# Performance work log

Measured on AMD Instinct MI355X. Metric: run time of the kernel, lower is better.

The kernel has to match this reference:

```python
import jax, jax.numpy as jnp
import numpy as np

B, DIN, DOUT, NC = 8192, 4096, 4096, 64


def setup_inputs() -> dict:
    key = jax.random.key(0)
    k1, k2, k3, k4, k5 = jax.random.split(key, 5)
    x = jax.random.normal(k1, (B, DIN), dtype=jnp.float32)
    cluster = jax.random.uniform(k2, (B, NC), dtype=jnp.float32)
    weight = jax.random.uniform(k3, (DIN, DOUT), dtype=jnp.float32,
                                minval=-0.25, maxval=0.25)
    # torch init is ones; perturb slightly so the modulation is non-trivial
    style_L = 1.0 + 0.1 * jax.random.normal(k4, (NC, DIN), dtype=jnp.float32)
    style_R = 1.0 + 0.1 * jax.random.normal(k5, (NC, DOUT), dtype=jnp.float32)
    return {"x": x, "cluster": cluster, "weight": weight,
            "style_L": style_L, "style_R": style_R}


def reference(x, cluster, weight, style_L, style_R):
    # tmp_L: (B, din), tmp_R: (B, dout)
    tmp_L = cluster @ style_L
    tmp_R = cluster @ style_R
    # Algebraically identical to (weight * outer(tmp_L, tmp_R)) applied per
    # sample: out[b,o] = sum_i x[b,i]*tmpL[b,i]*W[i,o]*tmpR[b,o].
    # Factorized form avoids the (B, din, dout) intermediate.
    return ((x * tmp_L) @ weight) * tmp_R
```

## Files before the change

### kernel.cpp

```cpp
#include <hip/hip_runtime.h>
#include <cstdint>

#define BB   8192
#define DIN  4096
#define DOUT 4096
#define NCL  64

typedef __bf16 bf16;
typedef __attribute__((ext_vector_type(8))) __bf16 bf16x8;
typedef __attribute__((ext_vector_type(4))) float   f32x4;

#define GAS(p) (reinterpret_cast<uint32_t __attribute__((address_space(1)))*>(reinterpret_cast<uintptr_t>(p)))
#define LAS(p) (reinterpret_cast<uint32_t __attribute__((address_space(3)))*>(reinterpret_cast<uintptr_t>(p)))

#define WAITV(n)  asm volatile("s_waitcnt vmcnt(" #n ")" ::: "memory")
#define WAITL()   asm volatile("s_waitcnt lgkmcnt(0)" ::: "memory")
#define BARR()    __builtin_amdgcn_s_barrier()
#define SCHED0()  __builtin_amdgcn_sched_barrier(0)
#define MFMA(a, b, c) __builtin_amdgcn_mfma_f32_16x16x32_bf16((a), (b), (c), 0, 0, 0)

__global__ __launch_bounds__(256) void prologue_kernel(
    const float* __restrict__ x, const float* __restrict__ cl,
    const float* __restrict__ sL, bf16* __restrict__ Ap,
    bf16* __restrict__ clb)
{
    __shared__ uint4 lds_u4[2048];
    char* lds = (char*)lds_u4;
    const int t    = threadIdx.x;
    const int lane = t & 63;
    const int w    = t >> 6;
    const int wm   = w >> 1, wn = w & 1;
    const int r0   = blockIdx.x * 128;
    const int c0   = blockIdx.y * 128;

    #pragma unroll
    for (int i = 0; i < 4; i++) {
        int tk  = t + i * 256;
        int row = tk >> 3, ch = tk & 7;
        const float* src = cl + (size_t)(r0 + row) * NCL + ch * 8;
        float4 v0 = *(const float4*)src;
        float4 v1 = *(const float4*)(src + 4);
        bf16x8 pk;
        pk[0]=(bf16)v0.x; pk[1]=(bf16)v0.y; pk[2]=(bf16)v0.z; pk[3]=(bf16)v0.w;
        pk[4]=(bf16)v1.x; pk[5]=(bf16)v1.y; pk[6]=(bf16)v1.z; pk[7]=(bf16)v1.w;
        *(bf16x8*)(lds + row * 128 + ((ch ^ (row & 7)) << 4)) = pk;
        if (blockIdx.y == 0)
            *(bf16x8*)(clb + (size_t)(r0 + row) * NCL + ch * 8) = pk;
    }
    #pragma unroll
    for (int i = 0; i < 4; i++) {
        int tk = t + i * 256;
        int n  = tk & 127, c = tk >> 7;
        bf16x8 pl;
        #pragma unroll
        for (int j = 0; j < 8; j++)
            pl[j] = (bf16)sL[(size_t)(c * 8 + j) * DIN + c0 + n];
        *(bf16x8*)(lds + 16384 + n * 128 + ((c ^ (n & 7)) << 4)) = pl;
    }
    __syncthreads();

    f32x4 accL[4][4] = {};
    #pragma unroll
    for (int s = 0; s < 2; s++) {
        bf16x8 a[4], bl[4];
        #pragma unroll
        for (int m = 0; m < 4; m++) {
            int row = wm * 64 + m * 16 + (lane & 15);
            int ch  = s * 4 + (lane >> 4);
            a[m] = *(bf16x8*)(lds + row * 128 + ((ch ^ (row & 7)) << 4));
        }
        #pragma unroll
        for (int n = 0; n < 4; n++) {
            int row = wn * 64 + n * 16 + (lane & 15);
            int ch  = s * 4 + (lane >> 4);
            bl[n] = *(bf16x8*)(lds + 16384 + row * 128 + ((ch ^ (row & 7)) << 4));
        }
        #pragma unroll
        for (int m = 0; m < 4; m++)
            #pragma unroll
            for (int n = 0; n < 4; n++)
                accL[m][n] = MFMA(a[m], bl[n], accL[m][n]);
    }

    #pragma unroll
    for (int m = 0; m < 4; m++) {
        int rbase = r0 + wm * 64 + m * 16 + ((lane >> 4) << 2);
        #pragma unroll
        for (int n = 0; n < 4; n++) {
            int col = c0 + wn * 64 + n * 16 + (lane & 15);
            #pragma unroll
            for (int j = 0; j < 4; j++) {
                size_t idx = (size_t)(rbase + j) * DIN + col;
                Ap[idx] = (bf16)(x[idx] * accL[m][n][j]);
            }
        }
    }
}

__global__ __launch_bounds__(256) void transpose_kernel(
    const float* __restrict__ W, bf16* __restrict__ Wt)
{
    const int t  = threadIdx.x;
    const int n  = blockIdx.x * 256 + t;
    const int k0 = blockIdx.y * 32;
    bf16x8 v[4];
    #pragma unroll
    for (int q = 0; q < 4; q++)
        #pragma unroll
        for (int j = 0; j < 8; j++)
            v[q][j] = (bf16)W[(size_t)(k0 + q * 8 + j) * DOUT + n];
    bf16* dst = Wt + (size_t)n * DIN + k0;
    #pragma unroll
    for (int q = 0; q < 4; q++)
        *(bf16x8*)(dst + q * 8) = v[q];
}

__global__ __launch_bounds__(256) void srt_kernel(
    const float* __restrict__ sR, bf16* __restrict__ srt)
{
    const int o = blockIdx.x * 256 + threadIdx.x;
    bf16x8 v[8];
    #pragma unroll
    for (int q = 0; q < 8; q++)
        #pragma unroll
        for (int j = 0; j < 8; j++)
            v[q][j] = (bf16)sR[(size_t)(q * 8 + j) * DOUT + o];
    bf16* dst = srt + (size_t)o * 64;
    #pragma unroll
    for (int q = 0; q < 8; q++)
        *(bf16x8*)(dst + q * 8) = v[q];
}

template<int CUR>
__device__ __forceinline__ void tile_step(char* lds, int tid,
    const bf16* pA1, const bf16* pA2, const bf16* pA3, const bf16* pA4,
    const bf16* pB1, const bf16* pB2, const bf16* pB3, const bf16* pB4,
    int kA1, int kA2, int aoff0, int aoff1, int boff0, int boff1,
    bf16x8 a[4][2], bf16x8 b[4][2], f32x4 acc[8][4])
{
    constexpr int CB = CUR * 65536;
    constexpr int OB = (CUR ^ 1) * 65536;

    #pragma unroll
    for (int mq = 0; mq < 4; ++mq) {
        a[mq][0] = *(const bf16x8*)(lds + CB + mq * 2048 + aoff0);
        a[mq][1] = *(const bf16x8*)(lds + CB + mq * 2048 + aoff1);
    }
    #pragma unroll
    for (int nb = 0; nb < 4; ++nb) {
        b[nb][0] = *(const bf16x8*)(lds + CB + nb * 2048 + boff0);
        b[nb][1] = *(const bf16x8*)(lds + CB + nb * 2048 + boff1);
    }
    __builtin_amdgcn_global_load_lds(GAS(pA3 + kA1), LAS(lds + OB + 16384 + tid * 16), 16, 0, 0);
    __builtin_amdgcn_global_load_lds(GAS(pA4 + kA1), LAS(lds + OB + 24576 + tid * 16), 16, 0, 0);
    BARR();
    WAITL(); SCHED0();
    __builtin_amdgcn_s_setprio(1);
    #pragma unroll
    for (int k = 0; k < 2; ++k)
        #pragma unroll
        for (int mq = 0; mq < 4; ++mq)
            #pragma unroll
            for (int nq = 0; nq < 2; ++nq)
                acc[mq][nq] = MFMA(a[mq][k], b[nq][k], acc[mq][nq]);
    __builtin_amdgcn_s_setprio(0);
    BARR();

    __builtin_amdgcn_global_load_lds(GAS(pB1 + kA2), LAS(lds + CB + 32768 + tid * 16), 16, 0, 0);
    __builtin_amdgcn_global_load_lds(GAS(pB2 + kA2), LAS(lds + CB + 40960 + tid * 16), 16, 0, 0);
    BARR();
    __builtin_amdgcn_s_setprio(1);
    #pragma unroll
    for (int k = 0; k < 2; ++k)
        #pragma unroll
        for (int mq = 0; mq < 4; ++mq)
            #pragma unroll
            for (int nq = 0; nq < 2; ++nq)
                acc[mq][2 + nq] = MFMA(a[mq][k], b[2 + nq][k], acc[mq][2 + nq]);
    __builtin_amdgcn_s_setprio(0);
    BARR();

    #pragma unroll
    for (int mq = 0; mq < 4; ++mq) {
        a[mq][0] = *(const bf16x8*)(lds + CB + 8192 + mq * 2048 + aoff0);
        a[mq][1] = *(const bf16x8*)(lds + CB + 8192 + mq * 2048 + aoff1);
    }
    __builtin_amdgcn_global_load_lds(GAS(pB3 + kA2), LAS(lds + CB + 49152 + tid * 16), 16, 0, 0);
    __builtin_amdgcn_global_load_lds(GAS(pB4 + kA2), LAS(lds + CB + 57344 + tid * 16), 16, 0, 0);
    BARR();
    WAITL(); SCHED0();
    __builtin_amdgcn_s_setprio(1);
    #pragma unroll
    for (int k = 0; k < 2; ++k)
        #pragma unroll
        for (int mq = 0; mq < 4; ++mq)
            #pragma unroll
            for (int nq = 0; nq < 2; ++nq)
                acc[4 + mq][2 + nq] = MFMA(a[mq][k], b[2 + nq][k], acc[4 + mq][2 + nq]);
    __builtin_amdgcn_s_setprio(0);
    BARR();

    __builtin_amdgcn_global_load_lds(GAS(pA1 + kA2), LAS(lds + CB + tid * 16), 16, 0, 0);
    __builtin_amdgcn_global_load_lds(GAS(pA2 + kA2), LAS(lds + CB + 8192 + tid * 16), 16, 0, 0);
    BARR();
    __builtin_amdgcn_s_setprio(1);
    #pragma unroll
    for (int k = 0; k < 2; ++k)
        #pragma unroll
        for (int mq = 0; mq < 4; ++mq)
            #pragma unroll
            for (int nq = 0; nq < 2; ++nq)
                acc[4 + mq][nq] = MFMA(a[mq][k], b[nq][k], acc[4 + mq][nq]);
    __builtin_amdgcn_s_setprio(0);
    WAITV(6);
    BARR();
}

__global__ __launch_bounds__(512, 2) void gemm_kernel(
    const bf16* __restrict__ Ap, const bf16* __restrict__ Wt,
    const bf16* __restrict__ clb, const bf16* __restrict__ srt,
    float* __restrict__ out)
{
    __shared__ uint4 smem[8192];
    char* lds = (char*)smem;
    const int tid  = threadIdx.x;
    const int lane = tid & 63;
    const int w    = tid >> 6;
    const int wm   = w >> 2;
    const int wn   = w & 3;
    const int L = lane & 15, H = lane >> 4;

    const int bid = blockIdx.x;
    const int xc  = bid & 7, ii = bid >> 3;
    const int mt  = xc * 4 + (ii >> 4);
    const int nt  = ii & 15;
    const size_t brow = (size_t)mt * 256;
    const size_t bcol = (size_t)nt * 256;

    const int r1  = tid >> 3;
    const int gch = (tid & 7) ^ (r1 & 7);
    const bf16* pA1 = Ap + (brow + r1) * (size_t)DIN + gch * 8;
    const bf16* pA2 = pA1 + (size_t)64  * DIN;
    const bf16* pA3 = pA1 + (size_t)128 * DIN;
    const bf16* pA4 = pA1 + (size_t)192 * DIN;
    const bf16* pB1 = Wt + (bcol + r1) * (size_t)DIN + gch * 8;
    const bf16* pB2 = pB1 + (size_t)64  * DIN;
    const bf16* pB3 = pB1 + (size_t)128 * DIN;
    const bf16* pB4 = pB1 + (size_t)192 * DIN;

    const int swz0 = (H ^ (L & 7)) << 4;
    const int swz1 = ((4 + H) ^ (L & 7)) << 4;
    const int aoff0 = wm * 16384 + L * 128 + swz0;
    const int aoff1 = wm * 16384 + L * 128 + swz1;
    const int boff0 = 32768 + (wn >> 1) * 16384 + (wn & 1) * 8192 + L * 128 + swz0;
    const int boff1 = 32768 + (wn >> 1) * 16384 + (wn & 1) * 8192 + L * 128 + swz1;

    bf16x8 a[4][2], b[4][2];
    f32x4 acc[8][4] = {};

    __builtin_amdgcn_global_load_lds(GAS(pA1), LAS(lds + tid * 16), 16, 0, 0);
    __builtin_amdgcn_global_load_lds(GAS(pA2), LAS(lds + 8192 + tid * 16), 16, 0, 0);
    __builtin_amdgcn_global_load_lds(GAS(pA3), LAS(lds + 16384 + tid * 16), 16, 0, 0);
    __builtin_amdgcn_global_load_lds(GAS(pA4), LAS(lds + 24576 + tid * 16), 16, 0, 0);
    __builtin_amdgcn_global_load_lds(GAS(pB1), LAS(lds + 32768 + tid * 16), 16, 0, 0);
    __builtin_amdgcn_global_load_lds(GAS(pB2), LAS(lds + 40960 + tid * 16), 16, 0, 0);
    __builtin_amdgcn_global_load_lds(GAS(pB3), LAS(lds + 49152 + tid * 16), 16, 0, 0);
    __builtin_amdgcn_global_load_lds(GAS(pB4), LAS(lds + 57344 + tid * 16), 16, 0, 0);
    __builtin_amdgcn_global_load_lds(GAS(pB1 + 64), LAS(lds + 65536 + 32768 + tid * 16), 16, 0, 0);
    __builtin_amdgcn_global_load_lds(GAS(pB2 + 64), LAS(lds + 65536 + 40960 + tid * 16), 16, 0, 0);
    __builtin_amdgcn_global_load_lds(GAS(pB3 + 64), LAS(lds + 65536 + 49152 + tid * 16), 16, 0, 0);
    __builtin_amdgcn_global_load_lds(GAS(pB4 + 64), LAS(lds + 65536 + 57344 + tid * 16), 16, 0, 0);
    __builtin_amdgcn_global_load_lds(GAS(pA1 + 64), LAS(lds + 65536 + tid * 16), 16, 0, 0);
    __builtin_amdgcn_global_load_lds(GAS(pA2 + 64), LAS(lds + 65536 + 8192 + tid * 16), 16, 0, 0);
    WAITV(6);
    BARR();

    #pragma unroll 1
    for (int t = 0; t < 64; t += 2) {
        tile_step<0>(lds, tid, pA1, pA2, pA3, pA4, pB1, pB2, pB3, pB4,
                     ((t + 1) & 63) * 64, ((t + 2) & 63) * 64,
                     aoff0, aoff1, boff0, boff1, a, b, acc);
        tile_step<1>(lds, tid, pA1, pA2, pA3, pA4, pB1, pB2, pB3, pB4,
                     ((t + 2) & 63) * 64, ((t + 3) & 63) * 64,
                     aoff0, aoff1, boff0, boff1, a, b, acc);
    }

    WAITV(0);
    const bf16* pC = clb + (brow + r1) * 64 + gch * 8;
    const bf16* pR = srt + (bcol + r1) * 64 + gch * 8;
    __builtin_amdgcn_global_load_lds(GAS(pC),         LAS(lds + tid * 16), 16, 0, 0);
    __builtin_amdgcn_global_load_lds(GAS(pC + 4096),  LAS(lds + 8192 + tid * 16), 16, 0, 0);
    __builtin_amdgcn_global_load_lds(GAS(pC + 8192),  LAS(lds + 16384 + tid * 16), 16, 0, 0);
    __builtin_amdgcn_global_load_lds(GAS(pC + 12288), LAS(lds + 24576 + tid * 16), 16, 0, 0);
    __builtin_amdgcn_global_load_lds(GAS(pR),         LAS(lds + 32768 + tid * 16), 16, 0, 0);
    __builtin_amdgcn_global_load_lds(GAS(pR + 4096),  LAS(lds + 40960 + tid * 16), 16, 0, 0);
    __builtin_amdgcn_global_load_lds(GAS(pR + 8192),  LAS(lds + 49152 + tid * 16), 16, 0, 0);
    __builtin_amdgcn_global_load_lds(GAS(pR + 12288), LAS(lds + 57344 + tid * 16), 16, 0, 0);
    WAITV(0);
    BARR();

    #pragma unroll
    for (int nb = 0; nb < 4; ++nb) {
        b[nb][0] = *(const bf16x8*)(lds + nb * 2048 + boff0);
        b[nb][1] = *(const bf16x8*)(lds + nb * 2048 + boff1);
    }
    #pragma unroll
    for (int half = 0; half < 2; ++half) {
        #pragma unroll
        for (int mq = 0; mq < 4; ++mq) {
            a[mq][0] = *(const bf16x8*)(lds + half * 8192 + mq * 2048 + aoff0);
            a[mq][1] = *(const bf16x8*)(lds + half * 8192 + mq * 2048 + aoff1);
        }
        WAITL(); SCHED0();
        f32x4 r4[4][4] = {};
        #pragma unroll
        for (int k = 0; k < 2; ++k)
            #pragma unroll
            for (int mq = 0; mq < 4; ++mq)
                #pragma unroll
                for (int nb = 0; nb < 4; ++nb)
                    r4[mq][nb] = MFMA(a[mq][k], b[nb][k], r4[mq][nb]);
        #pragma unroll
        for (int mq = 0; mq < 4; ++mq)
            #pragma unroll
            for (int nb = 0; nb < 4; ++nb)
                acc[half * 4 + mq][nb] *= r4[mq][nb];
    }

    #pragma unroll
    for (int m = 0; m < 8; m++) {
        size_t rbase = brow + (size_t)(wm * 128 + m * 16 + (H << 2));
        #pragma unroll
        for (int n = 0; n < 4; n++) {
            size_t col = bcol + (size_t)(wn * 64 + n * 16 + L);
            #pragma unroll
            for (int j = 0; j < 4; j++) {
                size_t idx = (rbase + j) * DOUT + col;
                out[idx] = acc[m][n][j];
            }
        }
    }
}

extern "C" void kernel_launch(void* const* d_in, const int* in_sizes, int n_in,
                              void* d_out, int out_size, void* d_ws, size_t ws_size,
                              hipStream_t stream)
{
    (void)in_sizes; (void)n_in; (void)out_size;
    const float* x  = (const float*)d_in[0];
    const float* cl = (const float*)d_in[1];
    const float* W  = (const float*)d_in[2];
    const float* sL = (const float*)d_in[3];
    const float* sR = (const float*)d_in[4];
    float* out = (float*)d_out;

    const size_t AP_BYTES = (size_t)BB * DIN * sizeof(bf16);
    const size_t WT_BYTES = (size_t)DIN * DOUT * sizeof(bf16);
    const size_t CL_BYTES = (size_t)BB * NCL * sizeof(bf16);
    const size_t SR_BYTES = (size_t)DOUT * NCL * sizeof(bf16);
    if (ws_size < AP_BYTES + WT_BYTES + CL_BYTES + SR_BYTES) return;

    char* ws = (char*)d_ws;
    bf16* Ap  = (bf16*)ws;
    bf16* Wt  = (bf16*)(ws + AP_BYTES);
    bf16* clb = (bf16*)(ws + AP_BYTES + WT_BYTES);
    bf16* srt = (bf16*)(ws + AP_BYTES + WT_BYTES + CL_BYTES);

    prologue_kernel<<<dim3(BB / 128, DIN / 128), 256, 0, stream>>>(x, cl, sL, Ap, clb);
    transpose_kernel<<<dim3(DOUT / 256, DIN / 32), 256, 0, stream>>>(W, Wt);
    srt_kernel<<<dim3(DOUT / 256), 256, 0, stream>>>(sR, srt);
    gemm_kernel<<<dim3((BB / 256) * (DOUT / 256)), 512, 0, stream>>>(Ap, Wt, clb, srt, out);
}
```

Baseline: 330.6 us.

## Merge prep kernels into one launch and split LDS waits in GEMM tile step

Folds the prologue, W transpose and style_R transpose kernels into a single prep kernel dispatched by block index, removing two launches and the gaps between them. Separately, the GEMM tile step reorders its LDS fragment reads and replaces full lgkmcnt(0) waits with partial counted waits, so the first half of the MFMAs can start while later fragments are still arriving. The counted waits rely on the exact order of LDS operations the compiler emits, and a wrong count would read stale registers. Mixing heterogeneous work in one grid may also change how well each part fills the GPU.

```diff
diff --git a/kernel.cpp b/kernel.cpp
--- a/kernel.cpp
+++ b/kernel.cpp
@@ -14,121 +14,119 @@
 #define LAS(p) (reinterpret_cast<uint32_t __attribute__((address_space(3)))*>(reinterpret_cast<uintptr_t>(p)))
 
 #define WAITV(n)  asm volatile("s_waitcnt vmcnt(" #n ")" ::: "memory")
-#define WAITL()   asm volatile("s_waitcnt lgkmcnt(0)" ::: "memory")
+#define WAITLN(n) asm volatile("s_waitcnt lgkmcnt(" #n ")" ::: "memory")
 #define BARR()    __builtin_amdgcn_s_barrier()
 #define SCHED0()  __builtin_amdgcn_sched_barrier(0)
 #define MFMA(a, b, c) __builtin_amdgcn_mfma_f32_16x16x32_bf16((a), (b), (c), 0, 0, 0)
 
-__global__ __launch_bounds__(256) void prologue_kernel(
+__global__ __launch_bounds__(256) void prep_kernel(
     const float* __restrict__ x, const float* __restrict__ cl,
-    const float* __restrict__ sL, bf16* __restrict__ Ap,
-    bf16* __restrict__ clb)
+    const float* __restrict__ sL, const float* __restrict__ sR,
+    const float* __restrict__ W,
+    bf16* __restrict__ Ap, bf16* __restrict__ clb,
+    bf16* __restrict__ Wt, bf16* __restrict__ srt)
 {
     __shared__ uint4 lds_u4[2048];
-    char* lds = (char*)lds_u4;
-    const int t    = threadIdx.x;
-    const int lane = t & 63;
-    const int w    = t >> 6;
-    const int wm   = w >> 1, wn = w & 1;
-    const int r0   = blockIdx.x * 128;
-    const int c0   = blockIdx.y * 128;
-
-    #pragma unroll
-    for (int i = 0; i < 4; i++) {
-        int tk  = t + i * 256;
-        int row = tk >> 3, ch = tk & 7;
-        const float* src = cl + (size_t)(r0 + row) * NCL + ch * 8;
-        float4 v0 = *(const float4*)src;
-        float4 v1 = *(const float4*)(src + 4);
-        bf16x8 pk;
-        pk[0]=(bf16)v0.x; pk[1]=(bf16)v0.y; pk[2]=(bf16)v0.z; pk[3]=(bf16)v0.w;
-        pk[4]=(bf16)v1.x; pk[5]=(bf16)v1.y; pk[6]=(bf16)v1.z; pk[7]=(bf16)v1.w;
-        *(bf16x8*)(lds + row * 128 + ((ch ^ (row & 7)) << 4)) = pk;
-        if (blockIdx.y == 0)
-            *(bf16x8*)(clb + (size_t)(r0 + row) * NCL + ch * 8) = pk;
-    }
-    #pragma unroll
-    for (int i = 0; i < 4; i++) {
-        int tk = t + i * 256;
-        int n  = tk & 127, c = tk >> 7;
-        bf16x8 pl;
-        #pragma unroll
-        for (int j = 0; j < 8; j++)
-            pl[j] = (bf16)sL[(size_t)(c * 8 + j) * DIN + c0 + n];
-        *(bf16x8*)(lds + 16384 + n * 128 + ((c ^ (n & 7)) << 4)) = pl;
-    }
-    __syncthreads();
-
-    f32x4 accL[4][4] = {};
-    #pragma unroll
-    for (int s = 0; s < 2; s++) {
-        bf16x8 a[4], bl[4];
+    const int bid = blockIdx.x;
+    const int t   = threadIdx.x;
+
+    if (bid < 2048) {
+        char* lds = (char*)lds_u4;
+        const int lane = t & 63;
+        const int w    = t >> 6;
+        const int wm   = w >> 1, wn = w & 1;
+        const int r0   = (bid & 63) * 128;
+        const int c0   = (bid >> 6) * 128;
+
+        #pragma unroll
+        for (int i = 0; i < 4; i++) {
+            int tk  = t + i * 256;
+            int row = tk >> 3, ch = tk & 7;
+            const float* src = cl + (size_t)(r0 + row) * NCL + ch * 8;
+            float4 v0 = *(const float4*)src;
+            float4 v1 = *(const float4*)(src + 4);
+            bf16x8 pk;
+            pk[0]=(bf16)v0.x; pk[1]=(bf16)v0.y; pk[2]=(bf16)v0.z; pk[3]=(bf16)v0.w;
+            pk[4]=(bf16)v1.x; pk[5]=(bf16)v1.y; pk[6]=(bf16)v1.z; pk[7]=(bf16)v1.w;
+            *(bf16x8*)(lds + row * 128 + ((ch ^ (row & 7)) << 4)) = pk;
+            if (bid < 64)
+                *(bf16x8*)(clb + (size_t)(r0 + row) * NCL + ch * 8) = pk;
+        }
+        #pragma unroll
+        for (int i = 0; i < 4; i++) {
+            int tk = t + i * 256;
+            int n  = tk & 127, c = tk >> 7;
+            bf16x8 pl;
+            #pragma unroll
+            for (int j = 0; j < 8; j++)
+                pl[j] = (bf16)sL[(size_t)(c * 8 + j) * DIN + c0 + n];
+            *(bf16x8*)(lds + 16384 + n * 128 + ((c ^ (n & 7)) << 4)) = pl;
+        }
+        __syncthreads();
+
+        f32x4 accL[4][4] = {};
+        #pragma unroll
+        for (int s = 0; s < 2; s++) {
+            bf16x8 a[4], bl[4];
+            #pragma unroll
+            for (int m = 0; m < 4; m++) {
+                int row = wm * 64 + m * 16 + (lane & 15);
+                int ch  = s * 4 + (lane >> 4);
+                a[m] = *(bf16x8*)(lds + row * 128 + ((ch ^ (row & 7)) << 4));
+            }
+            #pragma unroll
+            for (int n = 0; n < 4; n++) {
+                int row = wn * 64 + n * 16 + (lane & 15);
+                int ch  = s * 4 + (lane >> 4);
+                bl[n] = *(bf16x8*)(lds + 16384 + row * 128 + ((ch ^ (row & 7)) << 4));
+            }
+            #pragma unroll
+            for (int m = 0; m < 4; m++)
+                #pragma unroll
+                for (int n = 0; n < 4; n++)
+                    accL[m][n] = MFMA(a[m], bl[n], accL[m][n]);
+        }
+
         #pragma unroll
         for (int m = 0; m < 4; m++) {
-            int row = wm * 64 + m * 16 + (lane & 15);
-            int ch  = s * 4 + (lane >> 4);
-            a[m] = *(bf16x8*)(lds + row * 128 + ((ch ^ (row & 7)) << 4));
-        }
-        #pragma unroll
-        for (int n = 0; n < 4; n++) {
-            int row = wn * 64 + n * 16 + (lane & 15);
-            int ch  = s * 4 + (lane >> 4);
-            bl[n] = *(bf16x8*)(lds + 16384 + row * 128 + ((ch ^ (row & 7)) << 4));
-        }
-        #pragma unroll
-        for (int m = 0; m < 4; m++)
-            #pragma unroll
-            for (int n = 0; n < 4; n++)
-                accL[m][n] = MFMA(a[m], bl[n], accL[m][n]);
-    }
-
-    #pragma unroll
-    for (int m = 0; m < 4; m++) {
-        int rbase = r0 + wm * 64 + m * 16 + ((lane >> 4) << 2);
-        #pragma unroll
-        for (int n = 0; n < 4; n++) {
-            int col = c0 + wn * 64 + n * 16 + (lane & 15);
-            #pragma unroll
-            for (int j = 0; j < 4; j++) {
-                size_t idx = (size_t)(rbase + j) * DIN + col;
-                Ap[idx] = (bf16)(x[idx] * accL[m][n][j]);
+            int rbase = r0 + wm * 64 + m * 16 + ((lane >> 4) << 2);
+            #pragma unroll
+            for (int n = 0; n < 4; n++) {
+                int col = c0 + wn * 64 + n * 16 + (lane & 15);
+                #pragma unroll
+                for (int j = 0; j < 4; j++) {
+                    size_t idx = (size_t)(rbase + j) * DIN + col;
+                    Ap[idx] = (bf16)(x[idx] * accL[m][n][j]);
+                }
             }
         }
-    }
-}
-
-__global__ __launch_bounds__(256) void transpose_kernel(
-    const float* __restrict__ W, bf16* __restrict__ Wt)
-{
-    const int t  = threadIdx.x;
-    const int n  = blockIdx.x * 256 + t;
-    const int k0 = blockIdx.y * 32;
-    bf16x8 v[4];
-    #pragma unroll
-    for (int q = 0; q < 4; q++)
-        #pragma unroll
-        for (int j = 0; j < 8; j++)
-            v[q][j] = (bf16)W[(size_t)(k0 + q * 8 + j) * DOUT + n];
-    bf16* dst = Wt + (size_t)n * DIN + k0;
-    #pragma unroll
-    for (int q = 0; q < 4; q++)
-        *(bf16x8*)(dst + q * 8) = v[q];
-}
-
-__global__ __launch_bounds__(256) void srt_kernel(
-    const float* __restrict__ sR, bf16* __restrict__ srt)
-{
-    const int o = blockIdx.x * 256 + threadIdx.x;
-    bf16x8 v[8];
-    #pragma unroll
-    for (int q = 0; q < 8; q++)
-        #pragma unroll
-        for (int j = 0; j < 8; j++)
-            v[q][j] = (bf16)sR[(size_t)(q * 8 + j) * DOUT + o];
-    bf16* dst = srt + (size_t)o * 64;
-    #pragma unroll
-    for (int q = 0; q < 8; q++)
-        *(bf16x8*)(dst + q * 8) = v[q];
+    } else if (bid < 4096) {
+        const int tb = bid - 2048;
+        const int n  = (tb & 15) * 256 + t;
+        const int k0 = (tb >> 4) * 32;
+        bf16x8 v[4];
+        #pragma unroll
+        for (int q = 0; q < 4; q++)
+            #pragma unroll
+            for (int j = 0; j < 8; j++)
+                v[q][j] = (bf16)W[(size_t)(k0 + q * 8 + j) * DOUT + n];
+        bf16* dst = Wt + (size_t)n * DIN + k0;
+        #pragma unroll
+        for (int q = 0; q < 4; q++)
+            *(bf16x8*)(dst + q * 8) = v[q];
+    } else {
+        const int o = (bid - 4096) * 256 + t;
+        bf16x8 v[8];
+        #pragma unroll
+        for (int q = 0; q < 8; q++)
+            #pragma unroll
+            for (int j = 0; j < 8; j++)
+                v[q][j] = (bf16)sR[(size_t)(q * 8 + j) * DOUT + o];
+        bf16* dst = srt + (size_t)o * 64;
+        #pragma unroll
+        for (int q = 0; q < 8; q++)
+            *(bf16x8*)(dst + q * 8) = v[q];
+    }
 }
 
 template<int CUR>
@@ -142,33 +140,44 @@
     constexpr int OB = (CUR ^ 1) * 65536;
 
     #pragma unroll
-    for (int mq = 0; mq < 4; ++mq) {
+    for (int mq = 0; mq < 4; ++mq)
         a[mq][0] = *(const bf16x8*)(lds + CB + mq * 2048 + aoff0);
+    b[0][0] = *(const bf16x8*)(lds + CB + 0 * 2048 + boff0);
+    b[1][0] = *(const bf16x8*)(lds + CB + 1 * 2048 + boff0);
+    SCHED0();
+    #pragma unroll
+    for (int mq = 0; mq < 4; ++mq)
         a[mq][1] = *(const bf16x8*)(lds + CB + mq * 2048 + aoff1);
-    }
-    #pragma unroll
-    for (int nb = 0; nb < 4; ++nb) {
-        b[nb][0] = *(const bf16x8*)(lds + CB + nb * 2048 + boff0);
-        b[nb][1] = *(const bf16x8*)(lds + CB + nb * 2048 + boff1);
-    }
+    b[0][1] = *(const bf16x8*)(lds + CB + 0 * 2048 + boff1);
+    b[1][1] = *(const bf16x8*)(lds + CB + 1 * 2048 + boff1);
+    SCHED0();
+    b[2][0] = *(const bf16x8*)(lds + CB + 2 * 2048 + boff0);
+    b[3][0] = *(const bf16x8*)(lds + CB + 3 * 2048 + boff0);
+    b[2][1] = *(const bf16x8*)(lds + CB + 2 * 2048 + boff1);
+    b[3][1] = *(const bf16x8*)(lds + CB + 3 * 2048 + boff1);
     __builtin_amdgcn_global_load_lds(GAS(pA3 + kA1), LAS(lds + OB + 16384 + tid * 16), 16, 0, 0);
     __builtin_amdgcn_global_load_lds(GAS(pA4 + kA1), LAS(lds + OB + 24576 + tid * 16), 16, 0, 0);
     BARR();
-    WAITL(); SCHED0();
+    WAITLN(10); SCHED0();
     __builtin_amdgcn_s_setprio(1);
     #pragma unroll
-    for (int k = 0; k < 2; ++k)
-        #pragma unroll
-        for (int mq = 0; mq < 4; ++mq)
-            #pragma unroll
-            for (int nq = 0; nq < 2; ++nq)
-                acc[mq][nq] = MFMA(a[mq][k], b[nq][k], acc[mq][nq]);
+    for (int mq = 0; mq < 4; ++mq)
+        #pragma unroll
+        for (int nq = 0; nq < 2; ++nq)
+            acc[mq][nq] = MFMA(a[mq][0], b[nq][0], acc[mq][nq]);
+    WAITLN(4); SCHED0();
+    #pragma unroll
+    for (int mq = 0; mq < 4; ++mq)
+        #pragma unroll
+        for (int nq = 0; nq < 2; ++nq)
+            acc[mq][nq] = MFMA(a[mq][1], b[nq][1], acc[mq][nq]);
     __builtin_amdgcn_s_setprio(0);
     BARR();
 
     __builtin_amdgcn_global_load_lds(GAS(pB1 + kA2), LAS(lds + CB + 32768 + tid * 16), 16, 0, 0);
     __builtin_amdgcn_global_load_lds(GAS(pB2 + kA2), LAS(lds + CB + 40960 + tid * 16), 16, 0, 0);
     BARR();
+    WAITLN(0); SCHED0();
     __builtin_amdgcn_s_setprio(1);
     #pragma unroll
     for (int k = 0; k < 2; ++k)
@@ -181,22 +190,28 @@
     BARR();
 
     #pragma unroll
-    for (int mq = 0; mq < 4; ++mq) {
+    for (int mq = 0; mq < 4; ++mq)
         a[mq][0] = *(const bf16x8*)(lds + CB + 8192 + mq * 2048 + aoff0);
+    SCHED0();
+    #pragma unroll
+    for (int mq = 0; mq < 4; ++mq)
         a[mq][1] = *(const bf16x8*)(lds + CB + 8192 + mq * 2048 + aoff1);
-    }
     __builtin_amdgcn_global_load_lds(GAS(pB3 + kA2), LAS(lds + CB + 49152 + tid * 16), 16, 0, 0);
     __builtin_amdgcn_global_load_lds(GAS(pB4 + kA2), LAS(lds + CB + 57344 + tid * 16), 16, 0, 0);
     BARR();
-    WAITL(); SCHED0();
+    WAITLN(4); SCHED0();
     __builtin_amdgcn_s_setprio(1);
     #pragma unroll
-    for (int k = 0; k < 2; ++k)
-        #pragma unroll
-        for (int mq = 0; mq < 4; ++mq)
-            #pragma unroll
-            for (int nq = 0; nq < 2; ++nq)
-                acc[4 + mq][2 + nq] = MFMA(a[mq][k], b[2 + nq][k], acc[4 + mq][2 + nq]);
+    for (int mq = 0; mq < 4; ++mq)
+        #pragma unroll
+        for (int nq = 0; nq < 2; ++nq)
+            acc[4 + mq][2 + nq] = MFMA(a[mq][0], b[2 + nq][0], acc[4 + mq][2 + nq]);
+    WAITLN(0); SCHED0();
+    #pragma unroll
+    for (int mq = 0; mq < 4; ++mq)
+        #pragma unroll
+        for (int nq = 0; nq < 2; ++nq)
+            acc[4 + mq][2 + nq] = MFMA(a[mq][1], b[2 + nq][1], acc[4 + mq][2 + nq]);
     __builtin_amdgcn_s_setprio(0);
     BARR();
 
@@ -311,7 +326,7 @@
             a[mq][0] = *(const bf16x8*)(lds + half * 8192 + mq * 2048 + aoff0);
             a[mq][1] = *(const bf16x8*)(lds + half * 8192 + mq * 2048 + aoff1);
         }
-        WAITL(); SCHED0();
+        WAITLN(0); SCHED0();
         f32x4 r4[4][4] = {};
         #pragma unroll
         for (int k = 0; k < 2; ++k)
@@ -366,8 +381,6 @@
     bf16* clb = (bf16*)(ws + AP_BYTES + WT_BYTES);
     bf16* srt = (bf16*)(ws + AP_BYTES + WT_BYTES + CL_BYTES);
 
-    prologue_kernel<<<dim3(BB / 128, DIN / 128), 256, 0, stream>>>(x, cl, sL, Ap, clb);
-    transpose_kernel<<<dim3(DOUT / 256, DIN / 32), 256, 0, stream>>>(W, Wt);
-    srt_kernel<<<dim3(DOUT / 256), 256, 0, stream>>>(sR, srt);
+    prep_kernel<<<dim3(4112), 256, 0, stream>>>(x, cl, sL, sR, W, Ap, clb, Wt, srt);
     gemm_kernel<<<dim3((BB / 256) * (DOUT / 256)), 512, 0, stream>>>(Ap, Wt, clb, srt, out);
 }
```

Result: slower. 385.4 us (+16.6%).

## Coalesce prologue epilogue via LDS, split B fragment loads, remap block tiles

Applied to the files above, without the earlier changes.

The prologue epilogue now stages the tmp_L tile in LDS, then reads x and writes Ap with row-contiguous vector loads and stores instead of scattered scalar accesses. In the GEMM tile step, the second half of the B fragments is loaded from LDS just before it is needed, which lowers register pressure and overlaps those reads with the earlier MFMAs. The block-to-tile mapping changes so each XCD group covers an 8x8 block of tiles, which should improve L2 reuse. The extra LDS and barriers in the prologue cost some occupancy.

```diff
diff --git a/kernel.cpp b/kernel.cpp
--- a/kernel.cpp
+++ b/kernel.cpp
@@ -24,8 +24,7 @@
     const float* __restrict__ sL, bf16* __restrict__ Ap,
     bf16* __restrict__ clb)
 {
-    __shared__ uint4 lds_u4[2048];
-    char* lds = (char*)lds_u4;
+    __shared__ char lds[34816];
     const int t    = threadIdx.x;
     const int lane = t & 63;
     const int w    = t >> 6;
@@ -81,19 +80,35 @@
             for (int n = 0; n < 4; n++)
                 accL[m][n] = MFMA(a[m], bl[n], accL[m][n]);
     }
+    __syncthreads();
 
     #pragma unroll
     for (int m = 0; m < 4; m++) {
-        int rbase = r0 + wm * 64 + m * 16 + ((lane >> 4) << 2);
+        int rbase = wm * 64 + m * 16 + ((lane >> 4) << 2);
         #pragma unroll
         for (int n = 0; n < 4; n++) {
-            int col = c0 + wn * 64 + n * 16 + (lane & 15);
-            #pragma unroll
-            for (int j = 0; j < 4; j++) {
-                size_t idx = (size_t)(rbase + j) * DIN + col;
-                Ap[idx] = (bf16)(x[idx] * accL[m][n][j]);
-            }
-        }
+            int col = wn * 64 + n * 16 + (lane & 15);
+            #pragma unroll
+            for (int j = 0; j < 4; j++)
+                *(bf16*)(lds + (rbase + j) * 272 + col * 2) = (bf16)accL[m][n][j];
+        }
+    }
+    __syncthreads();
+
+    const int L = t & 15, H = (t >> 4) & 3;
+    #pragma unroll
+    for (int it = 0; it < 8; it++) {
+        int row = it * 16 + w * 4 + H;
+        bf16x8 tl = *(const bf16x8*)(lds + row * 272 + L * 16);
+        const float* xs = x + (size_t)(r0 + row) * DIN + c0 + L * 8;
+        float4 x0 = *(const float4*)xs;
+        float4 x1 = *(const float4*)(xs + 4);
+        bf16x8 o;
+        o[0]=(bf16)(x0.x*(float)tl[0]); o[1]=(bf16)(x0.y*(float)tl[1]);
+        o[2]=(bf16)(x0.z*(float)tl[2]); o[3]=(bf16)(x0.w*(float)tl[3]);
+        o[4]=(bf16)(x1.x*(float)tl[4]); o[5]=(bf16)(x1.y*(float)tl[5]);
+        o[6]=(bf16)(x1.z*(float)tl[6]); o[7]=(bf16)(x1.w*(float)tl[7]);
+        *(bf16x8*)(Ap + (size_t)(r0 + row) * DIN + c0 + L * 8) = o;
     }
 }
 
@@ -147,7 +162,7 @@
         a[mq][1] = *(const bf16x8*)(lds + CB + mq * 2048 + aoff1);
     }
     #pragma unroll
-    for (int nb = 0; nb < 4; ++nb) {
+    for (int nb = 0; nb < 2; ++nb) {
         b[nb][0] = *(const bf16x8*)(lds + CB + nb * 2048 + boff0);
         b[nb][1] = *(const bf16x8*)(lds + CB + nb * 2048 + boff1);
     }
@@ -166,9 +181,15 @@
     __builtin_amdgcn_s_setprio(0);
     BARR();
 
+    #pragma unroll
+    for (int nb = 2; nb < 4; ++nb) {
+        b[nb][0] = *(const bf16x8*)(lds + CB + nb * 2048 + boff0);
+        b[nb][1] = *(const bf16x8*)(lds + CB + nb * 2048 + boff1);
+    }
     __builtin_amdgcn_global_load_lds(GAS(pB1 + kA2), LAS(lds + CB + 32768 + tid * 16), 16, 0, 0);
     __builtin_amdgcn_global_load_lds(GAS(pB2 + kA2), LAS(lds + CB + 40960 + tid * 16), 16, 0, 0);
     BARR();
+    WAITL(); SCHED0();
     __builtin_amdgcn_s_setprio(1);
     #pragma unroll
     for (int k = 0; k < 2; ++k)
@@ -232,8 +253,8 @@
 
     const int bid = blockIdx.x;
     const int xc  = bid & 7, ii = bid >> 3;
-    const int mt  = xc * 4 + (ii >> 4);
-    const int nt  = ii & 15;
+    const int mt  = (xc >> 1) * 8 + (ii >> 3);
+    const int nt  = (xc & 1) * 8 + (ii & 7);
     const size_t brow = (size_t)mt * 256;
     const size_t bcol = (size_t)nt * 256;
 
```

After: 320.8 us. -3.0%, faster.
